# Kernel optimization log

Hardware: AMD Instinct MI355X
Metric: run time of the kernel (lower is better)

Reference implementation:

```python
import jax, jax.numpy as jnp
import numpy as np

B, A, L, D, H = 8, 16, 80, 128, 6  # scenes, agents/scene, lanes/scene, feat dim, heads
LN_EPS = 1e-5


def _build_edges():
    hi_l, wi_l = [], []
    n_agt = B * A
    for b in range(B):
        ids = np.concatenate([np.arange(b * A, (b + 1) * A),
                              n_agt + np.arange(b * L, (b + 1) * L)])
        n = len(ids)
        hi_l.append(np.repeat(ids, n))  # 'd -> (d n)'
        wi_l.append(np.tile(ids, n))    # 'd -> (n d)'
    return (jnp.asarray(np.concatenate(hi_l), dtype=jnp.int32),
            jnp.asarray(np.concatenate(wi_l), dtype=jnp.int32))


def setup_inputs() -> dict:
    key = jax.random.key(0)
    ks = jax.random.split(key, 10)
    w = 0.05  # small init so exp(att) is well-behaved
    hi, wi = _build_edges()
    return {
        "agents": jax.random.normal(ks[0], (B * A, D), jnp.float32),
        "lanes": jax.random.normal(ks[1], (B * L, D), jnp.float32),
        "Wq": w * jax.random.normal(ks[2], (D, H * D), jnp.float32),
        "Wk": w * jax.random.normal(ks[3], (D, H * D), jnp.float32),
        "Wv": w * jax.random.normal(ks[4], (D, H * D), jnp.float32),
        "Wout1": w * jax.random.normal(ks[5], (H * D, D), jnp.float32),
        "Wout2": w * jax.random.normal(ks[6], (D, D), jnp.float32),
        "W1": w * jax.random.normal(ks[7], (D, D), jnp.float32),
        "ln_g": jnp.ones((D,), jnp.float32),
        "ln_b": jnp.zeros((D,), jnp.float32),
        "W2": w * jax.random.normal(ks[8], (D, D), jnp.float32),
        "hi": hi,
        "wi": wi,
    }


def _layernorm(x, g, b):
    mu = x.mean(-1, keepdims=True)
    var = ((x - mu) ** 2).mean(-1, keepdims=True)
    return (x - mu) * jax.lax.rsqrt(var + LN_EPS) * g + b


def reference(agents, lanes, Wq, Wk, Wv, Wout1, Wout2, W1, ln_g, ln_b, W2, hi, wi):
    nodes = jnp.concatenate([agents, lanes], axis=0)  # [N, D]
    N = nodes.shape[0]
    n_agt = agents.shape[0]
    scale = D ** -0.5

    src = nodes[hi]  # [E, D] (query side)
    dst = nodes[wi]  # [E, D] (key/value side)
    q = (src @ Wq).reshape(-1, H, D)
    k = (dst @ Wk).reshape(-1, H, D)
    v = jax.nn.relu(dst @ Wv).reshape(-1, H, D)

    att = jnp.einsum('ehd,ehd->eh', q, k) * scale          # [E, H]
    att = jnp.exp(att - att.max())                          # global-max-shifted exp (as in source)
    denom = jax.ops.segment_sum(att, hi, num_segments=N)    # [N, H]
    att = att / denom[hi]
    out = jax.ops.segment_sum(att[..., None] * v, hi, num_segments=N)  # [N, H, D]
    out = out.reshape(N, H * D)

    out = jax.nn.relu(out @ Wout1) @ Wout2                  # to_out
    h = _layernorm(nodes @ W1 + out, ln_g, ln_b)
    h = jax.nn.relu(h)
    h = h @ W2
    h = jax.nn.relu(h + nodes)                              # residual to pre-attention nodes
    return h[:n_agt]
```

## Files before the change

### kernel.cpp

```cpp
#include <hip/hip_runtime.h>
#include <math.h>

#define LN_EPS 1e-5f


__global__ __launch_bounds__(256) void k_qv(
    const float* __restrict__ agents, const float* __restrict__ lanes,
    const float* __restrict__ Wv, const float* __restrict__ Wq,
    const float* __restrict__ W1, float* __restrict__ V,
    float* __restrict__ Qb, float* __restrict__ base)
{
    __shared__ float As[128][68];
    __shared__ float Bs[128][68];

    const int tid = threadIdx.x;
    const int bid = blockIdx.x;

    const float* W;
    float* Out;
    int r0, wc0, wstride, dstride;
    bool dorelu = false;
    if (bid < 144) {
        const int br = bid % 12, bc = bid / 12;
        r0 = br * 64; W = Wv; wc0 = bc * 64; wstride = 768;
        Out = V; dstride = 768; dorelu = true;
    } else if (bid < 168) {
        const int idx = bid - 144;
        r0 = (idx & 1) * 64; W = Wq; wc0 = (idx >> 1) * 64; wstride = 768;
        Out = Qb; dstride = 768;
    } else {
        const int idx = bid - 168;
        r0 = (idx & 1) * 64; W = W1; wc0 = (idx >> 1) * 64; wstride = 128;
        Out = base; dstride = 128;
    }

    {
        const int row = tid >> 2, kv = tid & 3;
        const int gr = r0 + row;
        const float* src = (gr < 128) ? (agents + (size_t)gr * 128)
                                      : (lanes + (size_t)(gr - 128) * 128);
        #pragma unroll
        for (int j = 0; j < 8; ++j) {
            const int k0 = kv * 4 + j * 16;
            const float4 a = *(const float4*)(src + k0);
            As[k0 + 0][row] = a.x; As[k0 + 1][row] = a.y;
            As[k0 + 2][row] = a.z; As[k0 + 3][row] = a.w;
        }
    }
    {
        const int kr = tid >> 4, c4 = tid & 15;
        #pragma unroll
        for (int i = 0; i < 8; ++i) {
            const int k = kr + 16 * i;
            *(float4*)&Bs[k][c4 * 4] =
                *(const float4*)(W + (size_t)k * wstride + wc0 + c4 * 4);
        }
    }
    __syncthreads();

    const int tx = tid & 15, ty = tid >> 4;
    float acc[4][4] = {};
    #pragma unroll 8
    for (int k = 0; k < 128; ++k) {
        const float4 a = *(const float4*)&As[k][ty * 4];
        const float4 b = *(const float4*)&Bs[k][tx * 4];
        const float av[4] = {a.x, a.y, a.z, a.w};
        #pragma unroll
        for (int i = 0; i < 4; ++i) {
            acc[i][0] += av[i] * b.x; acc[i][1] += av[i] * b.y;
            acc[i][2] += av[i] * b.z; acc[i][3] += av[i] * b.w;
        }
    }
    #pragma unroll
    for (int i = 0; i < 4; ++i) {
        float4 v = make_float4(acc[i][0], acc[i][1], acc[i][2], acc[i][3]);
        if (dorelu) {
            v.x = fmaxf(v.x, 0.f); v.y = fmaxf(v.y, 0.f);
            v.z = fmaxf(v.z, 0.f); v.w = fmaxf(v.w, 0.f);
        }
        *(float4*)(Out + (size_t)(r0 + ty * 4 + i) * dstride + wc0 + tx * 4) = v;
    }
}

__global__ __launch_bounds__(512) void k_attn2(
    const float* __restrict__ agents, const float* __restrict__ lanes,
    const float* __restrict__ Wk, const float* __restrict__ V,
    const float* __restrict__ Qb, float* __restrict__ AO)
{
    __shared__ float Ns[96][132];
    __shared__ float Vh[96][68];
    __shared__ float Qs[16][132];
    __shared__ float Tt[16][132];
    __shared__ float Sm[16][100];
    __shared__ float Wc[32][132];

    const int tid = threadIdx.x;
    const int b = blockIdx.x;
    const int s = b / 12, r12 = b % 12;
    const int h = r12 >> 1, half = r12 & 1;

    #pragma unroll
    for (int ii = 0; ii < 6; ++ii) {
        const int idx = tid + ii * 512;
        const int n = idx >> 5, c4 = idx & 31;
        const float* src = (n < 16) ? (agents + (size_t)(s * 16 + n) * 128)
                                    : (lanes + (size_t)(s * 80 + n - 16) * 128);
        *(float4*)&Ns[n][c4 * 4] = *(const float4*)(src + c4 * 4);
    }
    #pragma unroll
    for (int ii = 0; ii < 3; ++ii) {
        const int idx = tid + ii * 512;
        const int n = idx >> 4, c4 = idx & 15;
        const int g = (n < 16) ? (s * 16 + n) : (128 + s * 80 + (n - 16));
        *(float4*)&Vh[n][c4 * 4] =
            *(const float4*)(V + (size_t)g * 768 + h * 128 + half * 64 + c4 * 4);
    }
    {
        const int r = tid >> 5, c4 = tid & 31;
        *(float4*)&Qs[r][c4 * 4] =
            *(const float4*)(Qb + (size_t)(s * 16 + r) * 768 + h * 128 + c4 * 4);
    }
    __syncthreads();

    const int r = tid >> 5, kc = tid & 31;
    for (int ck = 0; ck < 4; ++ck) {
        {
            const int i0 = tid * 2;
            #pragma unroll
            for (int ii = 0; ii < 2; ++ii) {
                const int idx = i0 + ii;
                const int row = idx >> 5, c4 = idx & 31;
                *(float4*)&Wc[row][c4 * 4] =
                    *(const float4*)(Wk + (size_t)(ck * 32 + row) * 768 +
                                     h * 128 + c4 * 4);
            }
        }
        __syncthreads();
        {
            float acc = 0.f;
            #pragma unroll 8
            for (int c4 = 0; c4 < 32; ++c4) {
                const float4 q = *(const float4*)&Qs[r][c4 * 4];
                const float4 w = *(const float4*)&Wc[kc][c4 * 4];
                acc += q.x * w.x + q.y * w.y + q.z * w.z + q.w * w.w;
            }
            Tt[r][ck * 32 + kc] = acc;
        }
        __syncthreads();
    }

    {
        const int i = r, jc = kc;
        float s0 = 0, s1 = 0, s2 = 0;
        #pragma unroll 4
        for (int kk = 0; kk < 32; ++kk) {
            const float4 t4 = *(const float4*)&Tt[i][kk * 4];
            const float4 a  = *(const float4*)&Ns[jc][kk * 4];
            const float4 bb = *(const float4*)&Ns[jc + 32][kk * 4];
            const float4 c  = *(const float4*)&Ns[jc + 64][kk * 4];
            s0 += t4.x*a.x  + t4.y*a.y  + t4.z*a.z  + t4.w*a.w;
            s1 += t4.x*bb.x + t4.y*bb.y + t4.z*bb.z + t4.w*bb.w;
            s2 += t4.x*c.x  + t4.y*c.y  + t4.z*c.z  + t4.w*c.w;
        }
        const float scale = 0.088388347648318447f;
        s0 *= scale; s1 *= scale; s2 *= scale;
        float m = fmaxf(fmaxf(s0, s1), s2);
        #pragma unroll
        for (int o = 16; o >= 1; o >>= 1) m = fmaxf(m, __shfl_xor(m, o, 32));
        const float e0 = __expf(s0 - m), e1 = __expf(s1 - m), e2 = __expf(s2 - m);
        float sum = e0 + e1 + e2;
        #pragma unroll
        for (int o = 16; o >= 1; o >>= 1) sum += __shfl_xor(sum, o, 32);
        const float inv = 1.0f / sum;
        Sm[i][jc]      = e0 * inv;
        Sm[i][jc + 32] = e1 * inv;
        Sm[i][jc + 64] = e2 * inv;
    }

    {
        const int i = r, d = kc;
        float o0 = 0, o1 = 0;
        #pragma unroll 4
        for (int j = 0; j < 96; ++j) {
            const float p = Sm[i][j];
            const float2 v = *(const float2*)&Vh[j][2 * d];
            o0 += p * v.x; o1 += p * v.y;
        }
        float* dst = AO + (size_t)(s * 16 + i) * 768 + h * 128 + half * 64 + 2 * d;
        *(float2*)dst = make_float2(o0, o1);
    }
}

__global__ __launch_bounds__(256) void k_f1w(
    const float* __restrict__ AO, const float* __restrict__ Wout1,
    float* __restrict__ y1p)
{
    __shared__ float As[64][68];
    __shared__ float Bs[64][68];

    const int tid = threadIdx.x;
    const int b = blockIdx.x;
    const int ks = b >> 2, quad = b & 3;
    const int m0 = (quad >> 1) * 64, n0 = (quad & 1) * 64;

    {
        const int row = tid >> 2, kq = tid & 3;
        #pragma unroll
        for (int j = 0; j < 4; ++j) {
            const int k0 = kq * 4 + j * 16;
            const float4 a =
                *(const float4*)(AO + (size_t)(m0 + row) * 768 + ks * 64 + k0);
            As[k0 + 0][row] = a.x; As[k0 + 1][row] = a.y;
            As[k0 + 2][row] = a.z; As[k0 + 3][row] = a.w;
        }
    }
    {
        const int kr = tid >> 4, c4 = tid & 15;
        #pragma unroll
        for (int i = 0; i < 4; ++i) {
            const int k = kr + 16 * i;
            *(float4*)&Bs[k][c4 * 4] =
                *(const float4*)(Wout1 + (size_t)(ks * 64 + k) * 128 + n0 + c4 * 4);
        }
    }
    __syncthreads();

    const int tx = tid & 15, ty = tid >> 4;
    float acc[4][4] = {};
    #pragma unroll 8
    for (int k = 0; k < 64; ++k) {
        const float4 a = *(const float4*)&As[k][ty * 4];
        const float4 bv = *(const float4*)&Bs[k][tx * 4];
        const float av[4] = {a.x, a.y, a.z, a.w};
        #pragma unroll
        for (int i = 0; i < 4; ++i) {
            acc[i][0] += av[i] * bv.x; acc[i][1] += av[i] * bv.y;
            acc[i][2] += av[i] * bv.z; acc[i][3] += av[i] * bv.w;
        }
    }
    float* dst = y1p + (size_t)ks * 16384 + (size_t)m0 * 128 + n0;
    #pragma unroll
    for (int i = 0; i < 4; ++i)
        *(float4*)(dst + (size_t)(ty * 4 + i) * 128 + tx * 4) =
            make_float4(acc[i][0], acc[i][1], acc[i][2], acc[i][3]);
}

__global__ __launch_bounds__(512) void k_f2(
    const float* __restrict__ y1p, const float* __restrict__ base,
    const float* __restrict__ agents, const float* __restrict__ Wout2,
    const float* __restrict__ ln_g, const float* __restrict__ ln_b,
    const float* __restrict__ W2, float* __restrict__ out)
{
    const int a = blockIdx.x;
    const int tid = threadIdx.x;
    __shared__ float y1s[128];
    __shared__ float nr[128];
    __shared__ float br[128];
    __shared__ float hb[128];
    __shared__ float ps[512];
    __shared__ float red[4];

    if (tid < 32) {
        float4 acc = make_float4(0,0,0,0);
        #pragma unroll
        for (int ks = 0; ks < 12; ++ks) {
            const float4 v =
                *(const float4*)(y1p + (size_t)ks * 16384 + (size_t)a * 128 + tid * 4);
            acc.x += v.x; acc.y += v.y; acc.z += v.z; acc.w += v.w;
        }
        y1s[tid * 4 + 0] = fmaxf(acc.x, 0.f); y1s[tid * 4 + 1] = fmaxf(acc.y, 0.f);
        y1s[tid * 4 + 2] = fmaxf(acc.z, 0.f); y1s[tid * 4 + 3] = fmaxf(acc.w, 0.f);
    } else if (tid < 64) {
        const int t = tid - 32;
        *(float4*)&nr[t * 4] = *(const float4*)(agents + (size_t)a * 128 + t * 4);
    } else if (tid < 96) {
        const int t = tid - 64;
        *(float4*)&br[t * 4] = *(const float4*)(base + (size_t)a * 128 + t * 4);
    }
    __syncthreads();

    const int d = tid & 127, g = tid >> 7;
    {
        const int k0 = g * 32;
        float p = 0.f;
        #pragma unroll 8
        for (int k = 0; k < 32; ++k)
            p += y1s[k0 + k] * Wout2[(size_t)(k0 + k) * 128 + d];
        ps[tid] = p;
    }
    __syncthreads();

    float tval = 0.f;
    if (tid < 128) tval = ps[d] + ps[128 + d] + ps[256 + d] + ps[384 + d] + br[d];
    float s1 = tval, s2 = tval * tval;
    #pragma unroll
    for (int o = 32; o >= 1; o >>= 1) { s1 += __shfl_xor(s1, o); s2 += __shfl_xor(s2, o); }
    if (tid < 128 && (tid & 63) == 0) {
        red[(tid >> 6) * 2] = s1; red[(tid >> 6) * 2 + 1] = s2;
    }
    __syncthreads();
    if (tid < 128) {
        const float S1 = red[0] + red[2], S2 = red[1] + red[3];
        const float mu  = S1 * (1.0f / 128.0f);
        const float var = S2 * (1.0f / 128.0f) - mu * mu;
        const float rin = rsqrtf(var + LN_EPS);
        hb[tid] = fmaxf((tval - mu) * rin * ln_g[tid] + ln_b[tid], 0.0f);
    }
    __syncthreads();

    {
        const int k0 = g * 32;
        float p = 0.f;
        #pragma unroll 8
        for (int k = 0; k < 32; ++k)
            p += hb[k0 + k] * W2[(size_t)(k0 + k) * 128 + d];
        ps[tid] = p;
    }
    __syncthreads();
    if (tid < 128)
        out[(size_t)a * 128 + d] =
            fmaxf(ps[d] + ps[128 + d] + ps[256 + d] + ps[384 + d] + nr[d], 0.0f);
}

extern "C" void kernel_launch(void* const* d_in, const int* in_sizes, int n_in,
                              void* d_out, int out_size, void* d_ws, size_t ws_size,
                              hipStream_t stream)
{
    const float* agents = (const float*)d_in[0];
    const float* lanes  = (const float*)d_in[1];
    const float* Wq     = (const float*)d_in[2];
    const float* Wk     = (const float*)d_in[3];
    const float* Wv     = (const float*)d_in[4];
    const float* Wout1  = (const float*)d_in[5];
    const float* Wout2  = (const float*)d_in[6];
    const float* W1     = (const float*)d_in[7];
    const float* ln_g   = (const float*)d_in[8];
    const float* ln_b   = (const float*)d_in[9];
    const float* W2     = (const float*)d_in[10];

    float* ws = (float*)d_ws;
    float* V    = ws;
    float* Qb   = V + 768 * 768;
    float* base = Qb + 128 * 768;
    float* AO   = base + 16384;
    float* y1p  = AO + 128 * 768;
    float* outp = (float*)d_out;

    k_qv   <<<172, 256, 0, stream>>>(agents, lanes, Wv, Wq, W1, V, Qb, base);
    k_attn2<<<96, 512, 0, stream>>>(agents, lanes, Wk, V, Qb, AO);
    k_f1w  <<<48, 256, 0, stream>>>(AO, Wout1, y1p);
    k_f2   <<<128, 512, 0, stream>>>(y1p, base, agents, Wout2, ln_g, ln_b, W2, outp);
}
```

Before: 107.9 us.

## Fuse four kernels into one cooperative mega-kernel with grid syncs

Replaces the four separate launches (QKV projection, attention, Wout1 split-K GEMM, final LN/MLP) with a single cooperative kernel of 128 blocks x 512 threads, using grid.sync between phases and a union of shared-memory layouts. The projection phase is retiled to 64x128 tiles with 512 threads and the Wout1 phase to 2x4 per-thread tiles so they fit the new block shape. The aim is to remove inter-kernel launch gaps and tail latency. In exchange, the large static shared allocation (about 117 KB) limits occupancy, each phase uses fewer blocks than before, and grid-wide barriers carry their own cost.

```diff
diff --git a/kernel.cpp b/kernel.cpp
--- a/kernel.cpp
+++ b/kernel.cpp
@@ -1,325 +1,317 @@
 #include <hip/hip_runtime.h>
+#include <hip/hip_cooperative_groups.h>
 #include <math.h>
 
+namespace cg = cooperative_groups;
+
 #define LN_EPS 1e-5f
 
 
-__global__ __launch_bounds__(256) void k_qv(
+struct SmemP0 { float Ast[128][64]; float Bst[128][132]; };
+struct SmemPA { float Ns[96][132]; float Vh[96][68]; float Qs[16][132];
+                float Tt[16][132]; float Sm[16][100]; float Wc[32][132]; };
+struct SmemPB { float As[64][68]; float Bs[64][68]; };
+struct SmemPC { float y1s[128]; float nr[128]; float br[128];
+                float hb[128]; float ps[512]; float red[4]; };
+
+__global__ __launch_bounds__(512) void mega(
     const float* __restrict__ agents, const float* __restrict__ lanes,
-    const float* __restrict__ Wv, const float* __restrict__ Wq,
-    const float* __restrict__ W1, float* __restrict__ V,
-    float* __restrict__ Qb, float* __restrict__ base)
+    const float* __restrict__ Wq, const float* __restrict__ Wk,
+    const float* __restrict__ Wv, const float* __restrict__ Wout1,
+    const float* __restrict__ Wout2, const float* __restrict__ W1,
+    const float* __restrict__ ln_g, const float* __restrict__ ln_b,
+    const float* __restrict__ W2, float* __restrict__ V,
+    float* __restrict__ Qb, float* __restrict__ base,
+    float* __restrict__ AO, float* __restrict__ y1p,
+    float* __restrict__ out)
 {
-    __shared__ float As[128][68];
-    __shared__ float Bs[128][68];
-
+    __shared__ __align__(16) char smem[119808];
+    cg::grid_group grid = cg::this_grid();
     const int tid = threadIdx.x;
     const int bid = blockIdx.x;
 
-    const float* W;
-    float* Out;
-    int r0, wc0, wstride, dstride;
-    bool dorelu = false;
-    if (bid < 144) {
-        const int br = bid % 12, bc = bid / 12;
-        r0 = br * 64; W = Wv; wc0 = bc * 64; wstride = 768;
-        Out = V; dstride = 768; dorelu = true;
-    } else if (bid < 168) {
-        const int idx = bid - 144;
-        r0 = (idx & 1) * 64; W = Wq; wc0 = (idx >> 1) * 64; wstride = 768;
-        Out = Qb; dstride = 768;
-    } else {
-        const int idx = bid - 168;
-        r0 = (idx & 1) * 64; W = W1; wc0 = (idx >> 1) * 64; wstride = 128;
-        Out = base; dstride = 128;
+    if (bid < 86) {
+        SmemP0& S = *reinterpret_cast<SmemP0*>(smem);
+        const float* W; float* Out;
+        int r0, wc0, wstride, dstride; bool dorelu = false;
+        if (bid < 72) {
+            const int rb = bid % 12, cb = bid / 12;
+            r0 = rb * 64; W = Wv; wc0 = cb * 128; wstride = 768;
+            Out = V; dstride = 768; dorelu = true;
+        } else if (bid < 84) {
+            const int idx = bid - 72;
+            r0 = (idx & 1) * 64; W = Wq; wc0 = (idx >> 1) * 128; wstride = 768;
+            Out = Qb; dstride = 768;
+        } else {
+            const int idx = bid - 84;
+            r0 = idx * 64; W = W1; wc0 = 0; wstride = 128;
+            Out = base; dstride = 128;
+        }
+
+        {
+            const int row = tid >> 3, kq = tid & 7;
+            const int gr = r0 + row;
+            const float* src = (gr < 128) ? (agents + (size_t)gr * 128)
+                                          : (lanes + (size_t)(gr - 128) * 128);
+            #pragma unroll
+            for (int j = 0; j < 4; ++j) {
+                const int k0 = kq * 4 + j * 32;
+                const float4 a = *(const float4*)(src + k0);
+                S.Ast[k0 + 0][row] = a.x; S.Ast[k0 + 1][row] = a.y;
+                S.Ast[k0 + 2][row] = a.z; S.Ast[k0 + 3][row] = a.w;
+            }
+        }
+        {
+            const int kr = tid >> 5, c4 = tid & 31;
+            #pragma unroll
+            for (int i = 0; i < 8; ++i) {
+                const int k = kr + 16 * i;
+                *(float4*)&S.Bst[k][c4 * 4] =
+                    *(const float4*)(W + (size_t)k * wstride + wc0 + c4 * 4);
+            }
+        }
+        __syncthreads();
+
+        const int tx = tid & 31, ty = tid >> 5;
+        float acc[4][4] = {};
+        #pragma unroll 8
+        for (int k = 0; k < 128; ++k) {
+            const float4 a = *(const float4*)&S.Ast[k][ty * 4];
+            const float4 b = *(const float4*)&S.Bst[k][tx * 4];
+            const float av[4] = {a.x, a.y, a.z, a.w};
+            #pragma unroll
+            for (int i = 0; i < 4; ++i) {
+                acc[i][0] += av[i] * b.x; acc[i][1] += av[i] * b.y;
+                acc[i][2] += av[i] * b.z; acc[i][3] += av[i] * b.w;
+            }
+        }
+        #pragma unroll
+        for (int i = 0; i < 4; ++i) {
+            float4 v = make_float4(acc[i][0], acc[i][1], acc[i][2], acc[i][3]);
+            if (dorelu) {
+                v.x = fmaxf(v.x, 0.f); v.y = fmaxf(v.y, 0.f);
+                v.z = fmaxf(v.z, 0.f); v.w = fmaxf(v.w, 0.f);
+            }
+            *(float4*)(Out + (size_t)(r0 + ty * 4 + i) * dstride + wc0 + tx * 4) = v;
+        }
     }
+    grid.sync();
+
+    if (bid < 96) {
+        SmemPA& S = *reinterpret_cast<SmemPA*>(smem);
+        const int s = bid / 12, r12 = bid % 12;
+        const int h = r12 >> 1, half = r12 & 1;
+
+        #pragma unroll
+        for (int ii = 0; ii < 6; ++ii) {
+            const int idx = tid + ii * 512;
+            const int n = idx >> 5, c4 = idx & 31;
+            const float* src = (n < 16) ? (agents + (size_t)(s * 16 + n) * 128)
+                                        : (lanes + (size_t)(s * 80 + n - 16) * 128);
+            *(float4*)&S.Ns[n][c4 * 4] = *(const float4*)(src + c4 * 4);
+        }
+        #pragma unroll
+        for (int ii = 0; ii < 3; ++ii) {
+            const int idx = tid + ii * 512;
+            const int n = idx >> 4, c4 = idx & 15;
+            const int g = (n < 16) ? (s * 16 + n) : (128 + s * 80 + (n - 16));
+            *(float4*)&S.Vh[n][c4 * 4] =
+                *(const float4*)(V + (size_t)g * 768 + h * 128 + half * 64 + c4 * 4);
+        }
+        {
+            const int r = tid >> 5, c4 = tid & 31;
+            *(float4*)&S.Qs[r][c4 * 4] =
+                *(const float4*)(Qb + (size_t)(s * 16 + r) * 768 + h * 128 + c4 * 4);
+        }
+        __syncthreads();
+
+        const int r = tid >> 5, kc = tid & 31;
+        for (int ck = 0; ck < 4; ++ck) {
+            {
+                const int i0 = tid * 2;
+                #pragma unroll
+                for (int ii = 0; ii < 2; ++ii) {
+                    const int idx = i0 + ii;
+                    const int row = idx >> 5, c4 = idx & 31;
+                    *(float4*)&S.Wc[row][c4 * 4] =
+                        *(const float4*)(Wk + (size_t)(ck * 32 + row) * 768 +
+                                         h * 128 + c4 * 4);
+                }
+            }
+            __syncthreads();
+            {
+                float acc = 0.f;
+                #pragma unroll 8
+                for (int c4 = 0; c4 < 32; ++c4) {
+                    const float4 q = *(const float4*)&S.Qs[r][c4 * 4];
+                    const float4 w = *(const float4*)&S.Wc[kc][c4 * 4];
+                    acc += q.x * w.x + q.y * w.y + q.z * w.z + q.w * w.w;
+                }
+                S.Tt[r][ck * 32 + kc] = acc;
+            }
+            __syncthreads();
+        }
+
+        {
+            const int i = r, jc = kc;
+            float s0 = 0, s1 = 0, s2 = 0;
+            #pragma unroll 4
+            for (int kk = 0; kk < 32; ++kk) {
+                const float4 t4 = *(const float4*)&S.Tt[i][kk * 4];
+                const float4 a  = *(const float4*)&S.Ns[jc][kk * 4];
+                const float4 bb = *(const float4*)&S.Ns[jc + 32][kk * 4];
+                const float4 c  = *(const float4*)&S.Ns[jc + 64][kk * 4];
+                s0 += t4.x*a.x  + t4.y*a.y  + t4.z*a.z  + t4.w*a.w;
+                s1 += t4.x*bb.x + t4.y*bb.y + t4.z*bb.z + t4.w*bb.w;
+                s2 += t4.x*c.x  + t4.y*c.y  + t4.z*c.z  + t4.w*c.w;
+            }
+            const float scale = 0.088388347648318447f;
+            s0 *= scale; s1 *= scale; s2 *= scale;
+            float m = fmaxf(fmaxf(s0, s1), s2);
+            #pragma unroll
+            for (int o = 16; o >= 1; o >>= 1) m = fmaxf(m, __shfl_xor(m, o, 32));
+            const float e0 = __expf(s0 - m), e1 = __expf(s1 - m), e2 = __expf(s2 - m);
+            float sum = e0 + e1 + e2;
+            #pragma unroll
+            for (int o = 16; o >= 1; o >>= 1) sum += __shfl_xor(sum, o, 32);
+            const float inv = 1.0f / sum;
+            S.Sm[i][jc]      = e0 * inv;
+            S.Sm[i][jc + 32] = e1 * inv;
+            S.Sm[i][jc + 64] = e2 * inv;
+        }
+
+        {
+            const int i = r, d = kc;
+            float o0 = 0, o1 = 0;
+            #pragma unroll 4
+            for (int j = 0; j < 96; ++j) {
+                const float p = S.Sm[i][j];
+                const float2 v = *(const float2*)&S.Vh[j][2 * d];
+                o0 += p * v.x; o1 += p * v.y;
+            }
+            float* dst = AO + (size_t)(s * 16 + i) * 768 + h * 128 + half * 64 + 2 * d;
+            *(float2*)dst = make_float2(o0, o1);
+        }
+    }
+    grid.sync();
+
+    if (bid < 48) {
+        SmemPB& S = *reinterpret_cast<SmemPB*>(smem);
+        const int ks = bid >> 2, quad = bid & 3;
+        const int m0 = (quad >> 1) * 64, n0 = (quad & 1) * 64;
+
+        {
+            const int row = tid >> 3, kq = tid & 7;
+            #pragma unroll
+            for (int j = 0; j < 2; ++j) {
+                const int k0 = kq * 4 + j * 32;
+                const float4 a =
+                    *(const float4*)(AO + (size_t)(m0 + row) * 768 + ks * 64 + k0);
+                S.As[k0 + 0][row] = a.x; S.As[k0 + 1][row] = a.y;
+                S.As[k0 + 2][row] = a.z; S.As[k0 + 3][row] = a.w;
+            }
+        }
+        {
+            const int kr = tid >> 4, c4 = tid & 15;
+            #pragma unroll
+            for (int i = 0; i < 2; ++i) {
+                const int k = kr + 32 * i;
+                *(float4*)&S.Bs[k][c4 * 4] =
+                    *(const float4*)(Wout1 + (size_t)(ks * 64 + k) * 128 + n0 + c4 * 4);
+            }
+        }
+        __syncthreads();
+
+        const int tx = tid & 15, ty = tid >> 4;
+        float acc[2][4] = {};
+        #pragma unroll 8
+        for (int k = 0; k < 64; ++k) {
+            const float2 a = *(const float2*)&S.As[k][ty * 2];
+            const float4 b = *(const float4*)&S.Bs[k][tx * 4];
+            acc[0][0] += a.x * b.x; acc[0][1] += a.x * b.y;
+            acc[0][2] += a.x * b.z; acc[0][3] += a.x * b.w;
+            acc[1][0] += a.y * b.x; acc[1][1] += a.y * b.y;
+            acc[1][2] += a.y * b.z; acc[1][3] += a.y * b.w;
+        }
+        float* dst = y1p + (size_t)ks * 16384 + (size_t)m0 * 128 + n0;
+        #pragma unroll
+        for (int rr = 0; rr < 2; ++rr)
+            *(float4*)(dst + (size_t)(ty * 2 + rr) * 128 + tx * 4) =
+                make_float4(acc[rr][0], acc[rr][1], acc[rr][2], acc[rr][3]);
+    }
+    grid.sync();
 
     {
-        const int row = tid >> 2, kv = tid & 3;
-        const int gr = r0 + row;
-        const float* src = (gr < 128) ? (agents + (size_t)gr * 128)
-                                      : (lanes + (size_t)(gr - 128) * 128);
-        #pragma unroll
-        for (int j = 0; j < 8; ++j) {
-            const int k0 = kv * 4 + j * 16;
-            const float4 a = *(const float4*)(src + k0);
-            As[k0 + 0][row] = a.x; As[k0 + 1][row] = a.y;
-            As[k0 + 2][row] = a.z; As[k0 + 3][row] = a.w;
-        }
+        SmemPC& S = *reinterpret_cast<SmemPC*>(smem);
+        const int a = bid;
+
+        if (tid < 32) {
+            float4 acc = make_float4(0, 0, 0, 0);
+            #pragma unroll
+            for (int ks = 0; ks < 12; ++ks) {
+                const float4 v = *(const float4*)(y1p + (size_t)ks * 16384 +
+                                                  (size_t)a * 128 + tid * 4);
+                acc.x += v.x; acc.y += v.y; acc.z += v.z; acc.w += v.w;
+            }
+            S.y1s[tid * 4 + 0] = fmaxf(acc.x, 0.f);
+            S.y1s[tid * 4 + 1] = fmaxf(acc.y, 0.f);
+            S.y1s[tid * 4 + 2] = fmaxf(acc.z, 0.f);
+            S.y1s[tid * 4 + 3] = fmaxf(acc.w, 0.f);
+        } else if (tid < 64) {
+            const int t = tid - 32;
+            *(float4*)&S.nr[t * 4] = *(const float4*)(agents + (size_t)a * 128 + t * 4);
+        } else if (tid < 96) {
+            const int t = tid - 64;
+            *(float4*)&S.br[t * 4] = *(const float4*)(base + (size_t)a * 128 + t * 4);
+        }
+        __syncthreads();
+
+        const int d = tid & 127, g = tid >> 7;
+        {
+            const int k0 = g * 32;
+            float p = 0.f;
+            #pragma unroll 8
+            for (int k = 0; k < 32; ++k)
+                p += S.y1s[k0 + k] * Wout2[(size_t)(k0 + k) * 128 + d];
+            S.ps[tid] = p;
+        }
+        __syncthreads();
+
+        float tval = 0.f;
+        if (tid < 128)
+            tval = S.ps[d] + S.ps[128 + d] + S.ps[256 + d] + S.ps[384 + d] + S.br[d];
+        float s1 = tval, s2 = tval * tval;
+        #pragma unroll
+        for (int o = 32; o >= 1; o >>= 1) {
+            s1 += __shfl_xor(s1, o); s2 += __shfl_xor(s2, o);
+        }
+        if (tid < 128 && (tid & 63) == 0) {
+            S.red[(tid >> 6) * 2] = s1; S.red[(tid >> 6) * 2 + 1] = s2;
+        }
+        __syncthreads();
+        if (tid < 128) {
+            const float S1 = S.red[0] + S.red[2], S2 = S.red[1] + S.red[3];
+            const float mu  = S1 * (1.0f / 128.0f);
+            const float var = S2 * (1.0f / 128.0f) - mu * mu;
+            const float rin = rsqrtf(var + LN_EPS);
+            S.hb[tid] = fmaxf((tval - mu) * rin * ln_g[tid] + ln_b[tid], 0.0f);
+        }
+        __syncthreads();
+
+        {
+            const int k0 = g * 32;
+            float p = 0.f;
+            #pragma unroll 8
+            for (int k = 0; k < 32; ++k)
+                p += S.hb[k0 + k] * W2[(size_t)(k0 + k) * 128 + d];
+            S.ps[tid] = p;
+        }
+        __syncthreads();
+        if (tid < 128)
+            out[(size_t)a * 128 + d] =
+                fmaxf(S.ps[d] + S.ps[128 + d] + S.ps[256 + d] + S.ps[384 + d] +
+                      S.nr[d], 0.0f);
     }
-    {
-        const int kr = tid >> 4, c4 = tid & 15;
-        #pragma unroll
-        for (int i = 0; i < 8; ++i) {
-            const int k = kr + 16 * i;
-            *(float4*)&Bs[k][c4 * 4] =
-                *(const float4*)(W + (size_t)k * wstride + wc0 + c4 * 4);
-        }
-    }
-    __syncthreads();
-
-    const int tx = tid & 15, ty = tid >> 4;
-    float acc[4][4] = {};
-    #pragma unroll 8
-    for (int k = 0; k < 128; ++k) {
-        const float4 a = *(const float4*)&As[k][ty * 4];
-        const float4 b = *(const float4*)&Bs[k][tx * 4];
-        const float av[4] = {a.x, a.y, a.z, a.w};
-        #pragma unroll
-        for (int i = 0; i < 4; ++i) {
-            acc[i][0] += av[i] * b.x; acc[i][1] += av[i] * b.y;
-            acc[i][2] += av[i] * b.z; acc[i][3] += av[i] * b.w;
-        }
-    }
-    #pragma unroll
-    for (int i = 0; i < 4; ++i) {
-        float4 v = make_float4(acc[i][0], acc[i][1], acc[i][2], acc[i][3]);
-        if (dorelu) {
-            v.x = fmaxf(v.x, 0.f); v.y = fmaxf(v.y, 0.f);
-            v.z = fmaxf(v.z, 0.f); v.w = fmaxf(v.w, 0.f);
-        }
-        *(float4*)(Out + (size_t)(r0 + ty * 4 + i) * dstride + wc0 + tx * 4) = v;
-    }
-}
-
-__global__ __launch_bounds__(512) void k_attn2(
-    const float* __restrict__ agents, const float* __restrict__ lanes,
-    const float* __restrict__ Wk, const float* __restrict__ V,
-    const float* __restrict__ Qb, float* __restrict__ AO)
-{
-    __shared__ float Ns[96][132];
-    __shared__ float Vh[96][68];
-    __shared__ float Qs[16][132];
-    __shared__ float Tt[16][132];
-    __shared__ float Sm[16][100];
-    __shared__ float Wc[32][132];
-
-    const int tid = threadIdx.x;
-    const int b = blockIdx.x;
-    const int s = b / 12, r12 = b % 12;
-    const int h = r12 >> 1, half = r12 & 1;
-
-    #pragma unroll
-    for (int ii = 0; ii < 6; ++ii) {
-        const int idx = tid + ii * 512;
-        const int n = idx >> 5, c4 = idx & 31;
-        const float* src = (n < 16) ? (agents + (size_t)(s * 16 + n) * 128)
-                                    : (lanes + (size_t)(s * 80 + n - 16) * 128);
-        *(float4*)&Ns[n][c4 * 4] = *(const float4*)(src + c4 * 4);
-    }
-    #pragma unroll
-    for (int ii = 0; ii < 3; ++ii) {
-        const int idx = tid + ii * 512;
-        const int n = idx >> 4, c4 = idx & 15;
-        const int g = (n < 16) ? (s * 16 + n) : (128 + s * 80 + (n - 16));
-        *(float4*)&Vh[n][c4 * 4] =
-            *(const float4*)(V + (size_t)g * 768 + h * 128 + half * 64 + c4 * 4);
-    }
-    {
-        const int r = tid >> 5, c4 = tid & 31;
-        *(float4*)&Qs[r][c4 * 4] =
-            *(const float4*)(Qb + (size_t)(s * 16 + r) * 768 + h * 128 + c4 * 4);
-    }
-    __syncthreads();
-
-    const int r = tid >> 5, kc = tid & 31;
-    for (int ck = 0; ck < 4; ++ck) {
-        {
-            const int i0 = tid * 2;
-            #pragma unroll
-            for (int ii = 0; ii < 2; ++ii) {
-                const int idx = i0 + ii;
-                const int row = idx >> 5, c4 = idx & 31;
-                *(float4*)&Wc[row][c4 * 4] =
-                    *(const float4*)(Wk + (size_t)(ck * 32 + row) * 768 +
-                                     h * 128 + c4 * 4);
-            }
-        }
-        __syncthreads();
-        {
-            float acc = 0.f;
-            #pragma unroll 8
-            for (int c4 = 0; c4 < 32; ++c4) {
-                const float4 q = *(const float4*)&Qs[r][c4 * 4];
-                const float4 w = *(const float4*)&Wc[kc][c4 * 4];
-                acc += q.x * w.x + q.y * w.y + q.z * w.z + q.w * w.w;
-            }
-            Tt[r][ck * 32 + kc] = acc;
-        }
-        __syncthreads();
-    }
-
-    {
-        const int i = r, jc = kc;
-        float s0 = 0, s1 = 0, s2 = 0;
-        #pragma unroll 4
-        for (int kk = 0; kk < 32; ++kk) {
-            const float4 t4 = *(const float4*)&Tt[i][kk * 4];
-            const float4 a  = *(const float4*)&Ns[jc][kk * 4];
-            const float4 bb = *(const float4*)&Ns[jc + 32][kk * 4];
-            const float4 c  = *(const float4*)&Ns[jc + 64][kk * 4];
-            s0 += t4.x*a.x  + t4.y*a.y  + t4.z*a.z  + t4.w*a.w;
-            s1 += t4.x*bb.x + t4.y*bb.y + t4.z*bb.z + t4.w*bb.w;
-            s2 += t4.x*c.x  + t4.y*c.y  + t4.z*c.z  + t4.w*c.w;
-        }
-        const float scale = 0.088388347648318447f;
-        s0 *= scale; s1 *= scale; s2 *= scale;
-        float m = fmaxf(fmaxf(s0, s1), s2);
-        #pragma unroll
-        for (int o = 16; o >= 1; o >>= 1) m = fmaxf(m, __shfl_xor(m, o, 32));
-        const float e0 = __expf(s0 - m), e1 = __expf(s1 - m), e2 = __expf(s2 - m);
-        float sum = e0 + e1 + e2;
-        #pragma unroll
-        for (int o = 16; o >= 1; o >>= 1) sum += __shfl_xor(sum, o, 32);
-        const float inv = 1.0f / sum;
-        Sm[i][jc]      = e0 * inv;
-        Sm[i][jc + 32] = e1 * inv;
-        Sm[i][jc + 64] = e2 * inv;
-    }
-
-    {
-        const int i = r, d = kc;
-        float o0 = 0, o1 = 0;
-        #pragma unroll 4
-        for (int j = 0; j < 96; ++j) {
-            const float p = Sm[i][j];
-            const float2 v = *(const float2*)&Vh[j][2 * d];
-            o0 += p * v.x; o1 += p * v.y;
-        }
-        float* dst = AO + (size_t)(s * 16 + i) * 768 + h * 128 + half * 64 + 2 * d;
-        *(float2*)dst = make_float2(o0, o1);
-    }
-}
-
-__global__ __launch_bounds__(256) void k_f1w(
-    const float* __restrict__ AO, const float* __restrict__ Wout1,
-    float* __restrict__ y1p)
-{
-    __shared__ float As[64][68];
-    __shared__ float Bs[64][68];
-
-    const int tid = threadIdx.x;
-    const int b = blockIdx.x;
-    const int ks = b >> 2, quad = b & 3;
-    const int m0 = (quad >> 1) * 64, n0 = (quad & 1) * 64;
-
-    {
-        const int row = tid >> 2, kq = tid & 3;
-        #pragma unroll
-        for (int j = 0; j < 4; ++j) {
-            const int k0 = kq * 4 + j * 16;
-            const float4 a =
-                *(const float4*)(AO + (size_t)(m0 + row) * 768 + ks * 64 + k0);
-            As[k0 + 0][row] = a.x; As[k0 + 1][row] = a.y;
-            As[k0 + 2][row] = a.z; As[k0 + 3][row] = a.w;
-        }
-    }
-    {
-        const int kr = tid >> 4, c4 = tid & 15;
-        #pragma unroll
-        for (int i = 0; i < 4; ++i) {
-            const int k = kr + 16 * i;
-            *(float4*)&Bs[k][c4 * 4] =
-                *(const float4*)(Wout1 + (size_t)(ks * 64 + k) * 128 + n0 + c4 * 4);
-        }
-    }
-    __syncthreads();
-
-    const int tx = tid & 15, ty = tid >> 4;
-    float acc[4][4] = {};
-    #pragma unroll 8
-    for (int k = 0; k < 64; ++k) {
-        const float4 a = *(const float4*)&As[k][ty * 4];
-        const float4 bv = *(const float4*)&Bs[k][tx * 4];
-        const float av[4] = {a.x, a.y, a.z, a.w};
-        #pragma unroll
-        for (int i = 0; i < 4; ++i) {
-            acc[i][0] += av[i] * bv.x; acc[i][1] += av[i] * bv.y;
-            acc[i][2] += av[i] * bv.z; acc[i][3] += av[i] * bv.w;
-        }
-    }
-    float* dst = y1p + (size_t)ks * 16384 + (size_t)m0 * 128 + n0;
-    #pragma unroll
-    for (int i = 0; i < 4; ++i)
-        *(float4*)(dst + (size_t)(ty * 4 + i) * 128 + tx * 4) =
-            make_float4(acc[i][0], acc[i][1], acc[i][2], acc[i][3]);
-}
-
-__global__ __launch_bounds__(512) void k_f2(
-    const float* __restrict__ y1p, const float* __restrict__ base,
-    const float* __restrict__ agents, const float* __restrict__ Wout2,
-    const float* __restrict__ ln_g, const float* __restrict__ ln_b,
-    const float* __restrict__ W2, float* __restrict__ out)
-{
-    const int a = blockIdx.x;
-    const int tid = threadIdx.x;
-    __shared__ float y1s[128];
-    __shared__ float nr[128];
-    __shared__ float br[128];
-    __shared__ float hb[128];
-    __shared__ float ps[512];
-    __shared__ float red[4];
-
-    if (tid < 32) {
-        float4 acc = make_float4(0,0,0,0);
-        #pragma unroll
-        for (int ks = 0; ks < 12; ++ks) {
-            const float4 v =
-                *(const float4*)(y1p + (size_t)ks * 16384 + (size_t)a * 128 + tid * 4);
-            acc.x += v.x; acc.y += v.y; acc.z += v.z; acc.w += v.w;
-        }
-        y1s[tid * 4 + 0] = fmaxf(acc.x, 0.f); y1s[tid * 4 + 1] = fmaxf(acc.y, 0.f);
-        y1s[tid * 4 + 2] = fmaxf(acc.z, 0.f); y1s[tid * 4 + 3] = fmaxf(acc.w, 0.f);
-    } else if (tid < 64) {
-        const int t = tid - 32;
-        *(float4*)&nr[t * 4] = *(const float4*)(agents + (size_t)a * 128 + t * 4);
-    } else if (tid < 96) {
-        const int t = tid - 64;
-        *(float4*)&br[t * 4] = *(const float4*)(base + (size_t)a * 128 + t * 4);
-    }
-    __syncthreads();
-
-    const int d = tid & 127, g = tid >> 7;
-    {
-        const int k0 = g * 32;
-        float p = 0.f;
-        #pragma unroll 8
-        for (int k = 0; k < 32; ++k)
-            p += y1s[k0 + k] * Wout2[(size_t)(k0 + k) * 128 + d];
-        ps[tid] = p;
-    }
-    __syncthreads();
-
-    float tval = 0.f;
-    if (tid < 128) tval = ps[d] + ps[128 + d] + ps[256 + d] + ps[384 + d] + br[d];
-    float s1 = tval, s2 = tval * tval;
-    #pragma unroll
-    for (int o = 32; o >= 1; o >>= 1) { s1 += __shfl_xor(s1, o); s2 += __shfl_xor(s2, o); }
-    if (tid < 128 && (tid & 63) == 0) {
-        red[(tid >> 6) * 2] = s1; red[(tid >> 6) * 2 + 1] = s2;
-    }
-    __syncthreads();
-    if (tid < 128) {
-        const float S1 = red[0] + red[2], S2 = red[1] + red[3];
-        const float mu  = S1 * (1.0f / 128.0f);
-        const float var = S2 * (1.0f / 128.0f) - mu * mu;
-        const float rin = rsqrtf(var + LN_EPS);
-        hb[tid] = fmaxf((tval - mu) * rin * ln_g[tid] + ln_b[tid], 0.0f);
-    }
-    __syncthreads();
-
-    {
-        const int k0 = g * 32;
-        float p = 0.f;
-        #pragma unroll 8
-        for (int k = 0; k < 32; ++k)
-            p += hb[k0 + k] * W2[(size_t)(k0 + k) * 128 + d];
-        ps[tid] = p;
-    }
-    __syncthreads();
-    if (tid < 128)
-        out[(size_t)a * 128 + d] =
-            fmaxf(ps[d] + ps[128 + d] + ps[256 + d] + ps[384 + d] + nr[d], 0.0f);
 }
 
 extern "C" void kernel_launch(void* const* d_in, const int* in_sizes, int n_in,
@@ -342,12 +334,15 @@
     float* V    = ws;
     float* Qb   = V + 768 * 768;
     float* base = Qb + 128 * 768;
-    float* AO   = base + 16384;
+    float* AO   = base + 128 * 128;
     float* y1p  = AO + 128 * 768;
     float* outp = (float*)d_out;
 
-    k_qv   <<<172, 256, 0, stream>>>(agents, lanes, Wv, Wq, W1, V, Qb, base);
-    k_attn2<<<96, 512, 0, stream>>>(agents, lanes, Wk, V, Qb, AO);
-    k_f1w  <<<48, 256, 0, stream>>>(AO, Wout1, y1p);
-    k_f2   <<<128, 512, 0, stream>>>(y1p, base, agents, Wout2, ln_g, ln_b, W2, outp);
+    void* args[] = {
+        (void*)&agents, (void*)&lanes, (void*)&Wq, (void*)&Wk, (void*)&Wv,
+        (void*)&Wout1, (void*)&Wout2, (void*)&W1, (void*)&ln_g, (void*)&ln_b,
+        (void*)&W2, (void*)&V, (void*)&Qb, (void*)&base, (void*)&AO,
+        (void*)&y1p, (void*)&outp
+    };
+    hipLaunchCooperativeKernel((void*)mega, dim3(128), dim3(512), args, 0, stream);
 }
```

After: 180.2 us. 67.1% more time.
